# Kernel tuning notes

Measured on AMD Instinct MI355X. Metric: run time of the kernel, lower is better.

## Reference

```python
import jax, jax.numpy as jnp
import numpy as np
from jax import lax

V_PATCH = (1, 4, 16, 64, 256, 1024)  # must end at L
RESI = 0.5    # quant_resi ratio inside Phi
BETA = 0.25
K_PHI = 4     # share_quant_resi


def _phi_indices():
    # PhiPartiallyShared tick lookup, resolved statically per scale
    K = K_PHI
    ticks = np.linspace(1/3/K, 1 - 1/3/K, K) if K == 4 else np.linspace(1/2/K, 1 - 1/2/K, K)
    SN = len(V_PATCH)
    return [int(np.argmin(np.abs(ticks - (si / (SN - 1) if SN > 1 else 0.0)))) for si in range(SN)]


def interp_linear(x, Lo):
    # torch F.interpolate(mode='linear', align_corners=False) on last axis of [B,C,Li]
    Li = x.shape[-1]
    if Li == Lo:
        return x
    pos = (jnp.arange(Lo, dtype=jnp.float32) + 0.5) * (Li / Lo) - 0.5
    pos = jnp.clip(pos, 0.0, Li - 1)
    lo = jnp.floor(pos).astype(jnp.int32)
    hi = jnp.minimum(lo + 1, Li - 1)
    w = pos - lo.astype(jnp.float32)
    return x[..., lo] * (1.0 - w) + x[..., hi] * w


def phi_apply(h, w, b):
    # Phi: h*(1-r) + Conv1d(ks=3,pad=1)(h)*r
    y = lax.conv_general_dilated(h, w, (1,), [(1, 1)], dimension_numbers=('NCH', 'OIH', 'NCH'))
    y = y + b[None, :, None]
    return h * (1.0 - RESI) + y * RESI


def reference(f_BCL, emb, phi_w, phi_b):
    f = f_BCL.astype(jnp.float32)
    B, C, L = f.shape
    f_ng = lax.stop_gradient(f)
    f_rest = f_ng
    f_hat = jnp.zeros_like(f_ng)
    SN = len(V_PATCH)
    pidx = _phi_indices()
    e_sq = jnp.sum(emb * emb, axis=1)  # [V]
    loss = jnp.float32(0.0)
    for si, pl in enumerate(V_PATCH):
        rest = interp_linear(f_rest, pl) if si != SN - 1 else f_rest
        z = rest.transpose(0, 2, 1).reshape(-1, C)              # [B*pl, C]
        d = jnp.sum(z * z, axis=1, keepdims=True) + e_sq - 2.0 * (z @ emb.T)  # [B*pl, V]
        idx = jnp.argmin(d, axis=1)
        h = emb[idx].reshape(B, pl, C).transpose(0, 2, 1)        # [B,C,pl]
        if si != SN - 1:
            h = interp_linear(h, L)
        h = phi_apply(h, phi_w[pidx[si]], phi_b[pidx[si]])
        f_hat = f_hat + h
        f_rest = f_rest - h
        loss = loss + BETA * jnp.mean((lax.stop_gradient(f_hat) - f) ** 2) \
                    + jnp.mean((f_hat - f_ng) ** 2)
    loss = loss / SN
    # straight-through estimator
    f_hat_st = lax.stop_gradient(f_hat) - f_ng + f
    return f_hat_st, loss


def setup_inputs() -> dict:
    key = jax.random.key(0)
    k1, k2, k3 = jax.random.split(key, 3)
    B, C, L, V = 32, 32, 1024, 4096
    f_BCL = jax.random.normal(k1, (B, C, L), dtype=jnp.float32)
    emb = jax.random.normal(k2, (V, C), dtype=jnp.float32)
    phi_w = jax.random.normal(k3, (K_PHI, C, C, 3), dtype=jnp.float32) * 0.05
    phi_b = jnp.zeros((K_PHI, C), dtype=jnp.float32)
    return {"f_BCL": f_BCL, "emb": emb, "phi_w": phi_w, "phi_b": phi_b}
```

## Files before the change

### kernel.cpp

```cpp
#include <hip/hip_runtime.h>
#include <stdint.h>

#define BDIM 32
#define CDIM 32
#define LDIM 1024
#define VDIM 4096
#define BCL (BDIM*CDIM*LDIM)

typedef _Float16 f16x8 __attribute__((ext_vector_type(8)));
typedef float f32x4 __attribute__((ext_vector_type(4)));

#define PIN_V(x) asm volatile("" : "+v"(x))

__device__ __forceinline__ unsigned long long pack_key(float bd, int bv) {
    unsigned u = __float_as_uint(bd);
    u = (u & 0x80000000u) ? ~u : (u | 0x80000000u);
    return ((unsigned long long)u << 32) | (unsigned)bv;
}

__global__ void init_kernel(const float* __restrict__ f, const float* __restrict__ emb,
                            float* __restrict__ f_rest, float* __restrict__ f_hat,
                            float* __restrict__ e_sq, float* __restrict__ loss_acc,
                            unsigned* __restrict__ done_ctr,
                            unsigned long long* __restrict__ keys, int nkeys) {
    int i = blockIdx.x * blockDim.x + threadIdx.x;
    if (i < BCL) { f_rest[i] = f[i]; f_hat[i] = 0.0f; }
    if (i < VDIM) {
        const float* e = emb + (size_t)i * CDIM;
        float s = 0.f;
#pragma unroll
        for (int k = 0; k < 32; ++k) { float v = e[k]; s = fmaf(v, v, s); }
        e_sq[i] = s;
    }
    if (i < nkeys) keys[i] = ~0ull;
    if (i == 0) { *loss_acc = 0.f; *done_ctr = 0u; }
}

__global__ __launch_bounds__(256) void vq_small(
    const float* __restrict__ src, const float* __restrict__ emb,
    _Float16* __restrict__ eh, _Float16* __restrict__ el, float* __restrict__ e_sq,
    unsigned long long* __restrict__ keys,
    float* __restrict__ loss_acc, unsigned* __restrict__ done_ctr,
    int lpl, int s, int NQ)
{
    const int bid = blockIdx.x, t = threadIdx.x;
    if (bid >= NQ) {
        if (bid == NQ && t == 0) { *loss_acc = 0.f; *done_ctr = 0u; }
        int i = (bid - NQ) * 256 + t;
        if (i < VDIM) {
            const float* e = emb + (size_t)i * 32;
            float ssum = 0.f;
#pragma unroll
            for (int k = 0; k < 32; ++k) {
                float v = e[k];
                ssum = fmaf(v, v, ssum);
                _Float16 h = (_Float16)v;
                float r = v - (float)h;
                eh[(size_t)i*32 + k] = (_Float16)(-2.0f) * h;
                el[(size_t)i*32 + k] = (_Float16)(-2.0f) * (_Float16)r;
            }
            e_sq[i] = ssum;
        }
        return;
    }

    const int pl = 1 << lpl;
    const int q = bid;
    const int b = q >> lpl, j = q & (pl - 1);
    const int col = j * s + (s >> 1) - 1;
    const float* p = src + b * (CDIM * LDIM) + col;
    float z[32];
#pragma unroll
    for (int c = 0; c < 32; ++c) z[c] = 0.5f * (p[c * LDIM] + p[c * LDIM + 1]);

    float bd = 3.4e38f; int bv = 0;
    const int vs = t * 16;
    for (int v = vs; v < vs + 16; ++v) {
        const float* e = emb + (size_t)v * 32;
        float ev[32];
#pragma unroll
        for (int c = 0; c < 32; ++c) ev[c] = e[c];
        float es = 0.f;
#pragma unroll
        for (int c = 0; c < 32; ++c) es = fmaf(ev[c], ev[c], es);
        float a = z[0] * ev[0];
#pragma unroll
        for (int c = 1; c < 32; ++c) a = fmaf(z[c], ev[c], a);
        float d = fmaf(a, -2.0f, es);
        if (d < bd) { bd = d; bv = v; }
    }

    unsigned long long key = pack_key(bd, bv);
#pragma unroll
    for (int m = 1; m < 64; m <<= 1) {
        unsigned long long o = __shfl_xor(key, m, 64); if (o < key) key = o;
    }
    __shared__ unsigned long long redk[4];
    if ((t & 63) == 0) redk[t >> 6] = key;
    __syncthreads();
    if (t == 0) {
        unsigned long long kk = redk[0];
#pragma unroll
        for (int m = 1; m < 4; ++m) if (redk[m] < kk) kk = redk[m];
        keys[q] = kk;
    }
}

__global__ __launch_bounds__(256) void vq_mfma(
    const _Float16* __restrict__ z_hi, const _Float16* __restrict__ z_lo,
    const _Float16* __restrict__ e_hi, const _Float16* __restrict__ e_lo,
    const float* __restrict__ e_sq, unsigned long long* __restrict__ keys,
    int NQ, int VC, int vchunks, int vsub)
{
    const int t = threadIdx.x;
    const int lane = t & 63;
    const int w = t >> 6;
    const int qg = blockIdx.x / vchunks;
    const int vc = blockIdx.x % vchunks;
    const int vb0 = vc * (vsub * VC);

    __shared__ __align__(16) _Float16 eh_ls[256*32];
    __shared__ __align__(16) _Float16 el_ls[256*32];
    __shared__ float esq_ls[256];

    const int fr = lane & 15;
    const int kq = lane >> 4;
    const int qbase = qg*256 + w*64;
    f16x8 ah[4], al[4];
#pragma unroll
    for (int tq = 0; tq < 4; ++tq) {
        int q = qbase + tq*16 + fr;
        ah[tq] = *(const f16x8*)(z_hi + (size_t)q*32 + kq*8);
        al[tq] = *(const f16x8*)(z_lo + (size_t)q*32 + kq*8);
    }

    float bd[4][4]; int bv[4][4];
#pragma unroll
    for (int tq = 0; tq < 4; ++tq)
#pragma unroll
        for (int i = 0; i < 4; ++i) { bd[tq][i] = 3.4e38f; bv[tq][i] = 0; }

    for (int sub = 0; sub < vsub; ++sub) {
        const int vb = vb0 + sub * VC;
        {
            const float4* sH = (const float4*)(e_hi + (size_t)vb*32);
            const float4* sL = (const float4*)(e_lo + (size_t)vb*32);
            float4* dH = (float4*)eh_ls; float4* dL = (float4*)el_ls;
            int n4 = VC * 4;
            for (int x = t; x < n4; x += 256) {
                int row = x >> 2, c = x & 3;
                int ds = row*4 + (c ^ ((row >> 1) & 3));
                dH[ds] = sH[x]; dL[ds] = sL[x];
            }
            for (int v = t; v < VC; v += 256) esq_ls[v] = e_sq[vb + v];
        }
        __syncthreads();

        for (int vt = 0; vt < VC; vt += 16) {
            const int row = vt + fr;
            const int koff = (kq ^ ((row >> 1) & 3)) * 8;
            const f16x8 bh = *(const f16x8*)(eh_ls + (size_t)row*32 + koff);
            const f16x8 bl = *(const f16x8*)(el_ls + (size_t)row*32 + koff);
            float es = esq_ls[row];
            int vg = vb + row;
#pragma unroll
            for (int tq = 0; tq < 4; ++tq) {
                f32x4 acc = {es, es, es, es};
                acc = __builtin_amdgcn_mfma_f32_16x16x32_f16(ah[tq], bh, acc, 0,0,0);
                acc = __builtin_amdgcn_mfma_f32_16x16x32_f16(ah[tq], bl, acc, 0,0,0);
                acc = __builtin_amdgcn_mfma_f32_16x16x32_f16(al[tq], bh, acc, 0,0,0);
#pragma unroll
                for (int i = 0; i < 4; ++i)
                    if (acc[i] < bd[tq][i]) { bd[tq][i] = acc[i]; bv[tq][i] = vg; }
            }
        }
        __syncthreads();
    }

#pragma unroll
    for (int tq = 0; tq < 4; ++tq) {
#pragma unroll
        for (int i = 0; i < 4; ++i) {
            unsigned long long k = pack_key(bd[tq][i], bv[tq][i]);
#pragma unroll
            for (int m = 1; m < 16; m <<= 1) {
                unsigned long long o = __shfl_xor(k, m, 64); if (o < k) k = o;
            }
            if (fr == 0) atomicMin(&keys[qbase + tq*16 + kq*4 + i], k);
        }
    }
}

__global__ __launch_bounds__(256) void vq_scan(
    const float* __restrict__ f_rest,
    const float* __restrict__ emb, const float* __restrict__ e_sq,
    unsigned long long* __restrict__ keys,
    int lpl, int s, int NQ, int VC, int vchunks)
{
    const int pl = 1 << lpl;
    const int t  = threadIdx.x;
    const int qg = blockIdx.x / vchunks;
    const int vc = blockIdx.x % vchunks;
    const int vb = vc * VC;

    __shared__ __align__(16) float e_ls[128 * 32];
    __shared__ float esq_ls[128];

    {
        const float4* src = (const float4*)emb + (size_t)vb * 8;
        float4* dst = (float4*)e_ls;
        for (int x = t; x < VC * 8; x += 256) dst[x] = src[x];
        if (t < VC) esq_ls[t] = e_sq[vb + t];
    }

    const int q0 = qg * 512 + t;
    const int q1 = q0 + 256;
    const int qc0 = (q0 < NQ) ? q0 : NQ - 1;
    const int qc1 = (q1 < NQ) ? q1 : NQ - 1;

    float z0[32], z1[32];
    {
        int b0 = qc0 >> lpl, j0 = qc0 & (pl - 1);
        int b1 = qc1 >> lpl, j1 = qc1 & (pl - 1);
        if (pl == LDIM) {
            const float* p0 = f_rest + b0 * (CDIM * LDIM) + j0;
            const float* p1 = f_rest + b1 * (CDIM * LDIM) + j1;
#pragma unroll
            for (int c = 0; c < 32; ++c) { z0[c] = p0[c * LDIM]; z1[c] = p1[c * LDIM]; }
        } else {
            int col0 = j0 * s + (s >> 1) - 1;
            int col1 = j1 * s + (s >> 1) - 1;
            const float* p0 = f_rest + b0 * (CDIM * LDIM) + col0;
            const float* p1 = f_rest + b1 * (CDIM * LDIM) + col1;
#pragma unroll
            for (int c = 0; c < 32; ++c) {
                z0[c] = 0.5f * (p0[c * LDIM] + p0[c * LDIM + 1]);
                z1[c] = 0.5f * (p1[c * LDIM] + p1[c * LDIM + 1]);
            }
        }
    }

    __syncthreads();

    float bd0 = 3.4e38f, bd1 = 3.4e38f;
    int bv0 = 0, bv1 = 0;

#pragma unroll 1
    for (int v = 0; v < VC; v += 2) {
#pragma unroll
        for (int c = 0; c < 32; ++c) { PIN_V(z0[c]); PIN_V(z1[c]); }

        const float4* er0 = (const float4*)&e_ls[(size_t)v * 32];
        const float4* er1 = er0 + 8;
        float es0 = esq_ls[v];
        float es1 = esq_ls[v + 1];

        float4 e0 = er0[0], e1 = er1[0];
        float a00 = z0[0] * e0.x,        a01 = z0[0] * e1.x;
        float a10 = z1[0] * e0.x,        a11 = z1[0] * e1.x;
        a00 = fmaf(z0[1], e0.y, a00);    a01 = fmaf(z0[1], e1.y, a01);
        a10 = fmaf(z1[1], e0.y, a10);    a11 = fmaf(z1[1], e1.y, a11);
        a00 = fmaf(z0[2], e0.z, a00);    a01 = fmaf(z0[2], e1.z, a01);
        a10 = fmaf(z1[2], e0.z, a10);    a11 = fmaf(z1[2], e1.z, a11);
        a00 = fmaf(z0[3], e0.w, a00);    a01 = fmaf(z0[3], e1.w, a01);
        a10 = fmaf(z1[3], e0.w, a10);    a11 = fmaf(z1[3], e1.w, a11);
#pragma unroll
        for (int c4 = 1; c4 < 8; ++c4) {
            e0 = er0[c4]; e1 = er1[c4];
            a00 = fmaf(z0[c4*4+0], e0.x, a00);  a01 = fmaf(z0[c4*4+0], e1.x, a01);
            a10 = fmaf(z1[c4*4+0], e0.x, a10);  a11 = fmaf(z1[c4*4+0], e1.x, a11);
            a00 = fmaf(z0[c4*4+1], e0.y, a00);  a01 = fmaf(z0[c4*4+1], e1.y, a01);
            a10 = fmaf(z1[c4*4+1], e0.y, a10);  a11 = fmaf(z1[c4*4+1], e1.y, a11);
            a00 = fmaf(z0[c4*4+2], e0.z, a00);  a01 = fmaf(z0[c4*4+2], e1.z, a01);
            a10 = fmaf(z1[c4*4+2], e0.z, a10);  a11 = fmaf(z1[c4*4+2], e1.z, a11);
            a00 = fmaf(z0[c4*4+3], e0.w, a00);  a01 = fmaf(z0[c4*4+3], e1.w, a01);
            a10 = fmaf(z1[c4*4+3], e0.w, a10);  a11 = fmaf(z1[c4*4+3], e1.w, a11);
        }
        float d00 = fmaf(a00, -2.0f, es0);
        float d01 = fmaf(a01, -2.0f, es1);
        float d10 = fmaf(a10, -2.0f, es0);
        float d11 = fmaf(a11, -2.0f, es1);
        if (d00 < bd0) { bd0 = d00; bv0 = vb + v; }
        if (d01 < bd0) { bd0 = d01; bv0 = vb + v + 1; }
        if (d10 < bd1) { bd1 = d10; bv1 = vb + v; }
        if (d11 < bd1) { bd1 = d11; bv1 = vb + v + 1; }
    }

    if (q0 < NQ) atomicMin(&keys[q0], pack_key(bd0, bv0));
    if (q1 < NQ) atomicMin(&keys[q1], pack_key(bd1, bv1));
}

__global__ __launch_bounds__(256) void fuse_kernel(
    const float* __restrict__ f, const float* __restrict__ emb,
    const unsigned long long* __restrict__ keys,
    unsigned long long* __restrict__ keys_next, int nq_next,
    _Float16* __restrict__ zh_next, _Float16* __restrict__ zl_next, int s_next,
    const float* __restrict__ w, const float* __restrict__ bias,
    float* __restrict__ f_rest, float* __restrict__ f_hat,
    float* __restrict__ loss_acc, unsigned* __restrict__ done_ctr,
    float* __restrict__ out_loss, int pl, int from_f)
{
    const int t  = threadIdx.x;
    const int b  = blockIdx.y;
    const int l0 = blockIdx.x * 64;

    if (keys_next) {
        int x = (b * gridDim.x + blockIdx.x) * 256 + t;
        if (x < nq_next) keys_next[x] = ~0ull;
    }

    __shared__ float w_s[3072];
    __shared__ float b_s[32];
    __shared__ float hs[32 * 68];
    __shared__ float red[4];
    __shared__ int   v0s[66], v1s[66];
    __shared__ float wgs[66];

    for (int x = t; x < 3072; x += 256) w_s[x] = w[x];
    if (t < 32) b_s[t] = bias[t];

    if (t < 66) {
        int l = l0 - 1 + t;
        if (l < 0 || l >= LDIM) {
            v0s[t] = -1;
        } else {
            int lo, hi; float wg;
            if (pl == LDIM) { lo = l; hi = l; wg = 0.f; }
            else {
                float pos = (l + 0.5f) * ((float)pl / 1024.0f) - 0.5f;
                pos = fminf(fmaxf(pos, 0.f), (float)(pl - 1));
                lo = (int)floorf(pos);
                hi = min(lo + 1, pl - 1);
                wg = pos - (float)lo;
            }
            v0s[t] = (int)(keys[b * pl + lo] & 0xFFFFFFFFull);
            v1s[t] = (int)(keys[b * pl + hi] & 0xFFFFFFFFull);
            wgs[t] = wg;
        }
    }
    __syncthreads();

    for (int x = t; x < 528; x += 256) {
        int cx = x >> 3, i4 = x & 7;
        int v0 = v0s[cx];
        if (v0 < 0) {
            hs[(i4*4+0) * 68 + cx] = 0.f;
            hs[(i4*4+1) * 68 + cx] = 0.f;
            hs[(i4*4+2) * 68 + cx] = 0.f;
            hs[(i4*4+3) * 68 + cx] = 0.f;
        } else {
            float4 a = ((const float4*)(emb + (size_t)v0 * 32))[i4];
            float4 c = ((const float4*)(emb + (size_t)v1s[cx] * 32))[i4];
            float wg = wgs[cx], om = 1.0f - wg;
            hs[(i4*4+0) * 68 + cx] = a.x * om + c.x * wg;
            hs[(i4*4+1) * 68 + cx] = a.y * om + c.y * wg;
            hs[(i4*4+2) * 68 + cx] = a.z * om + c.z * wg;
            hs[(i4*4+3) * 68 + cx] = a.w * om + c.w * wg;
        }
    }
    __syncthreads();

    const int o  = t >> 3;
    const int lg = t & 7;
    const float* wrow = &w_s[o * 96];
    float acc[8];
#pragma unroll
    for (int u = 0; u < 8; ++u) acc[u] = 0.f;
    const int hbase = lg * 8;

#pragma unroll 2
    for (int i = 0; i < 32; ++i) {
        float w0 = wrow[i * 3 + 0], w1 = wrow[i * 3 + 1], w2 = wrow[i * 3 + 2];
        const float* hrow = &hs[i * 68 + hbase];
        float hw[10];
#pragma unroll
        for (int x = 0; x < 10; ++x) hw[x] = hrow[x];
#pragma unroll
        for (int u = 0; u < 8; ++u) {
            acc[u] = fmaf(w0, hw[u], acc[u]);
            acc[u] = fmaf(w1, hw[u + 1], acc[u]);
            acc[u] = fmaf(w2, hw[u + 2], acc[u]);
        }
    }

    float lsum = 0.f;
    float frv[8];
    const int gbase = (b * 32 + o) * LDIM + l0 + lg * 8;
#pragma unroll
    for (int u = 0; u < 8; ++u) {
        float hval = hs[o * 68 + lg * 8 + 1 + u];
        float y = acc[u] + b_s[o];
        float ph = 0.5f * hval + 0.5f * y;
        int gi = gbase + u;
        float fv = f[gi];
        float fh = (from_f ? 0.0f : f_hat[gi]) + ph;
        f_hat[gi] = fh;
        float fr = (from_f ? fv : f_rest[gi]) - ph;
        f_rest[gi] = fr;
        frv[u] = fr;
        float df = fh - fv;
        lsum = fmaf(df, df, lsum);
    }

    if (zh_next) {
        __syncthreads();
#pragma unroll
        for (int u = 0; u < 8; ++u) hs[o * 68 + lg * 8 + u] = frv[u];
        __syncthreads();
        int npos = 64 / s_next;
        int qn_base = b * (LDIM / s_next) + l0 / s_next;
        for (int v = t; v < npos * 32; v += 256) {
            int jl = v >> 5, c = v & 31;
            float zv;
            if (s_next == 1) zv = hs[c * 68 + jl];
            else {
                int cl = jl * s_next + (s_next >> 1) - 1;
                zv = 0.5f * (hs[c * 68 + cl] + hs[c * 68 + cl + 1]);
            }
            _Float16 h = (_Float16)zv;
            float r = zv - (float)h;
            size_t zi = (size_t)(qn_base + jl) * 32 + c;
            zh_next[zi] = h;
            zl_next[zi] = (_Float16)r;
        }
    }

#pragma unroll
    for (int off = 32; off > 0; off >>= 1) lsum += __shfl_down(lsum, off, 64);
    if ((t & 63) == 0) red[t >> 6] = lsum;
    __syncthreads();
    if (t == 0) {
        atomicAdd(loss_acc, red[0] + red[1] + red[2] + red[3]);
        if (out_loss) {
            __threadfence();
            unsigned old = atomicAdd(done_ctr, 1u);
            if (old == (unsigned)(gridDim.x * gridDim.y - 1)) {
                float lv = atomicAdd(loss_acc, 0.0f);
                *out_loss = lv * (1.25f / (6.0f * (float)BCL));
            }
        }
    }
}

extern "C" void kernel_launch(void* const* d_in, const int* in_sizes, int n_in,
                              void* d_out, int out_size, void* d_ws, size_t ws_size,
                              hipStream_t stream)
{
    const float* f    = (const float*)d_in[0];
    const float* emb  = (const float*)d_in[1];
    const float* phiw = (const float*)d_in[2];
    const float* phib = (const float*)d_in[3];

    float* f_hat    = (float*)d_out;
    float* out_loss = f_hat + BCL;

    const int pls[6]   = {1, 4, 16, 64, 256, 1024};
    const int lpls[6]  = {0, 2, 4, 6, 8, 10};
    const int vchm[6]  = {0, 0, 64, 16, 8, 4};
    const int vsbm[6]  = {0, 0, 1, 1, 2, 4};
    const int pidx[6]  = {0, 0, 1, 2, 3, 3};
    const int snx[6]   = {256, 64, 16, 4, 1, 0};

    char* ws = (char*)d_ws;
    float* f_rest = (float*)ws;

    size_t base = (size_t)BCL * 4;
    size_t off = base;
    unsigned long long* keysA = (unsigned long long*)(ws + off);
    unsigned long long* keysB = keysA + 32768;
    off += (size_t)65536 * 8;
    _Float16* z_hi = (_Float16*)(ws + off); off += (size_t)32768 * 32 * 2;
    _Float16* z_lo = (_Float16*)(ws + off); off += (size_t)32768 * 32 * 2;
    _Float16* e_hi = (_Float16*)(ws + off); off += (size_t)VDIM * 32 * 2;
    _Float16* e_lo = (_Float16*)(ws + off); off += (size_t)VDIM * 32 * 2;
    size_t need_mf = off + (size_t)VDIM * 4 + 64;
    bool mf = ws_size >= need_mf;

    if (mf) {
        float* e_sq        = (float*)(ws + off);
        float* loss_acc    = e_sq + VDIM;
        unsigned* done_ctr = (unsigned*)(loss_acc + 1);

        for (int si = 0; si < 6; ++si) {
            int pl = pls[si], s = LDIM / pl, NQ = BDIM * pl;
            unsigned long long* k  = (si & 1) ? keysB : keysA;
            unsigned long long* kn = (si >= 1 && si < 5) ? ((si & 1) ? keysA : keysB) : nullptr;
            int nq_next = (si < 5) ? BDIM * pls[si + 1] : 0;

            if (si <= 1) {
                int grid = NQ + (si == 0 ? 16 : 0);
                vq_small<<<dim3(grid), 256, 0, stream>>>(
                    (si == 0) ? f : f_rest, emb, e_hi, e_lo, e_sq, k,
                    loss_acc, done_ctr, lpls[si], s, NQ);
            } else {
                int vcm = vchm[si], vsb = vsbm[si];
                int VC = VDIM / (vcm * vsb);
                vq_mfma<<<dim3((NQ / 256) * vcm), 256, 0, stream>>>(
                    z_hi, z_lo, e_hi, e_lo, e_sq, k, NQ, VC, vcm, vsb);
            }

            bool zw = (si >= 1 && si <= 4);
            fuse_kernel<<<dim3(16, 32), 256, 0, stream>>>(
                f, emb, k, kn, nq_next,
                zw ? z_hi : nullptr, zw ? z_lo : nullptr, snx[si],
                phiw + (size_t)pidx[si] * 3072, phib + (size_t)pidx[si] * 32,
                f_rest, f_hat, loss_acc, done_ctr,
                (si == 5) ? out_loss : nullptr, pl, (si == 0) ? 1 : 0);
        }
        return;
    }

    {
        const int vch[6]  = {64, 64, 64, 64, 32, 32};
        off = base;
        size_t need_pp = base + (size_t)65536 * 8 + (size_t)VDIM * 4 + 64;
        bool pp = ws_size >= need_pp;
        keysB = pp ? keysA + 32768 : keysA;
        off += pp ? (size_t)65536 * 8 : (size_t)32768 * 8;
        float* e_sq        = (float*)(ws + off);
        float* loss_acc    = e_sq + VDIM;
        unsigned* done_ctr = (unsigned*)(loss_acc + 1);

        init_kernel<<<dim3((BCL + 255) / 256), 256, 0, stream>>>(
            f, emb, f_rest, f_hat, e_sq, loss_acc, done_ctr, keysA, 32768);

        for (int si = 0; si < 6; ++si) {
            int pl = pls[si], s = LDIM / pl, NQ = BDIM * pl;
            int qgroups = (NQ + 511) >> 9;
            int VC = VDIM / vch[si];
            unsigned long long* k  = (si & 1) ? keysB : keysA;
            unsigned long long* kn = (si < 5 && pp) ? ((si & 1) ? keysA : keysB) : nullptr;
            int nq_next = (si < 5) ? BDIM * pls[si + 1] : 0;
            if (!pp && si > 0) hipMemsetAsync(k, 0xFF, (size_t)NQ * 8, stream);
            vq_scan<<<dim3(qgroups * vch[si]), 256, 0, stream>>>(
                f_rest, emb, e_sq, k, lpls[si], s, NQ, VC, vch[si]);
            fuse_kernel<<<dim3(16, 32), 256, 0, stream>>>(
                f, emb, k, kn, nq_next, nullptr, nullptr, snx[si],
                phiw + (size_t)pidx[si] * 3072, phib + (size_t)pidx[si] * 32,
                f_rest, f_hat, loss_acc, done_ctr,
                (si == 5) ? out_loss : nullptr, pl, 0);
        }
    }
}
```

Baseline: 332.1 us.

## Drop f_hat tracking via f-minus-residual identity and shrink fuse tile

Stops carrying f_hat through every scale. The code now relies on f_hat = f - f_rest, so the loss uses the residual squared, and f_hat is written only once in the final scale instead of being read and written at every scale. The fuse kernel is templated on chunk width, and most scales use 16-column chunks with a 4x larger grid for more parallelism. The fallback path replaces vq_scan with vq_small. In exchange, the narrower tiles reload weights per block and add halo overhead, and the loss now relies on the algebraic identity holding in float arithmetic.

```diff
diff --git a/kernel.cpp b/kernel.cpp
--- a/kernel.cpp
+++ b/kernel.cpp
@@ -19,12 +19,12 @@
 }
 
 __global__ void init_kernel(const float* __restrict__ f, const float* __restrict__ emb,
-                            float* __restrict__ f_rest, float* __restrict__ f_hat,
+                            float* __restrict__ f_rest,
                             float* __restrict__ e_sq, float* __restrict__ loss_acc,
                             unsigned* __restrict__ done_ctr,
                             unsigned long long* __restrict__ keys, int nkeys) {
     int i = blockIdx.x * blockDim.x + threadIdx.x;
-    if (i < BCL) { f_rest[i] = f[i]; f_hat[i] = 0.0f; }
+    if (i < BCL) f_rest[i] = f[i];
     if (i < VDIM) {
         const float* e = emb + (size_t)i * CDIM;
         float s = 0.f;
@@ -191,105 +191,7 @@
     }
 }
 
-__global__ __launch_bounds__(256) void vq_scan(
-    const float* __restrict__ f_rest,
-    const float* __restrict__ emb, const float* __restrict__ e_sq,
-    unsigned long long* __restrict__ keys,
-    int lpl, int s, int NQ, int VC, int vchunks)
-{
-    const int pl = 1 << lpl;
-    const int t  = threadIdx.x;
-    const int qg = blockIdx.x / vchunks;
-    const int vc = blockIdx.x % vchunks;
-    const int vb = vc * VC;
-
-    __shared__ __align__(16) float e_ls[128 * 32];
-    __shared__ float esq_ls[128];
-
-    {
-        const float4* src = (const float4*)emb + (size_t)vb * 8;
-        float4* dst = (float4*)e_ls;
-        for (int x = t; x < VC * 8; x += 256) dst[x] = src[x];
-        if (t < VC) esq_ls[t] = e_sq[vb + t];
-    }
-
-    const int q0 = qg * 512 + t;
-    const int q1 = q0 + 256;
-    const int qc0 = (q0 < NQ) ? q0 : NQ - 1;
-    const int qc1 = (q1 < NQ) ? q1 : NQ - 1;
-
-    float z0[32], z1[32];
-    {
-        int b0 = qc0 >> lpl, j0 = qc0 & (pl - 1);
-        int b1 = qc1 >> lpl, j1 = qc1 & (pl - 1);
-        if (pl == LDIM) {
-            const float* p0 = f_rest + b0 * (CDIM * LDIM) + j0;
-            const float* p1 = f_rest + b1 * (CDIM * LDIM) + j1;
-#pragma unroll
-            for (int c = 0; c < 32; ++c) { z0[c] = p0[c * LDIM]; z1[c] = p1[c * LDIM]; }
-        } else {
-            int col0 = j0 * s + (s >> 1) - 1;
-            int col1 = j1 * s + (s >> 1) - 1;
-            const float* p0 = f_rest + b0 * (CDIM * LDIM) + col0;
-            const float* p1 = f_rest + b1 * (CDIM * LDIM) + col1;
-#pragma unroll
-            for (int c = 0; c < 32; ++c) {
-                z0[c] = 0.5f * (p0[c * LDIM] + p0[c * LDIM + 1]);
-                z1[c] = 0.5f * (p1[c * LDIM] + p1[c * LDIM + 1]);
-            }
-        }
-    }
-
-    __syncthreads();
-
-    float bd0 = 3.4e38f, bd1 = 3.4e38f;
-    int bv0 = 0, bv1 = 0;
-
-#pragma unroll 1
-    for (int v = 0; v < VC; v += 2) {
-#pragma unroll
-        for (int c = 0; c < 32; ++c) { PIN_V(z0[c]); PIN_V(z1[c]); }
-
-        const float4* er0 = (const float4*)&e_ls[(size_t)v * 32];
-        const float4* er1 = er0 + 8;
-        float es0 = esq_ls[v];
-        float es1 = esq_ls[v + 1];
-
-        float4 e0 = er0[0], e1 = er1[0];
-        float a00 = z0[0] * e0.x,        a01 = z0[0] * e1.x;
-        float a10 = z1[0] * e0.x,        a11 = z1[0] * e1.x;
-        a00 = fmaf(z0[1], e0.y, a00);    a01 = fmaf(z0[1], e1.y, a01);
-        a10 = fmaf(z1[1], e0.y, a10);    a11 = fmaf(z1[1], e1.y, a11);
-        a00 = fmaf(z0[2], e0.z, a00);    a01 = fmaf(z0[2], e1.z, a01);
-        a10 = fmaf(z1[2], e0.z, a10);    a11 = fmaf(z1[2], e1.z, a11);
-        a00 = fmaf(z0[3], e0.w, a00);    a01 = fmaf(z0[3], e1.w, a01);
-        a10 = fmaf(z1[3], e0.w, a10);    a11 = fmaf(z1[3], e1.w, a11);
-#pragma unroll
-        for (int c4 = 1; c4 < 8; ++c4) {
-            e0 = er0[c4]; e1 = er1[c4];
-            a00 = fmaf(z0[c4*4+0], e0.x, a00);  a01 = fmaf(z0[c4*4+0], e1.x, a01);
-            a10 = fmaf(z1[c4*4+0], e0.x, a10);  a11 = fmaf(z1[c4*4+0], e1.x, a11);
-            a00 = fmaf(z0[c4*4+1], e0.y, a00);  a01 = fmaf(z0[c4*4+1], e1.y, a01);
-            a10 = fmaf(z1[c4*4+1], e0.y, a10);  a11 = fmaf(z1[c4*4+1], e1.y, a11);
-            a00 = fmaf(z0[c4*4+2], e0.z, a00);  a01 = fmaf(z0[c4*4+2], e1.z, a01);
-            a10 = fmaf(z1[c4*4+2], e0.z, a10);  a11 = fmaf(z1[c4*4+2], e1.z, a11);
-            a00 = fmaf(z0[c4*4+3], e0.w, a00);  a01 = fmaf(z0[c4*4+3], e1.w, a01);
-            a10 = fmaf(z1[c4*4+3], e0.w, a10);  a11 = fmaf(z1[c4*4+3], e1.w, a11);
-        }
-        float d00 = fmaf(a00, -2.0f, es0);
-        float d01 = fmaf(a01, -2.0f, es1);
-        float d10 = fmaf(a10, -2.0f, es0);
-        float d11 = fmaf(a11, -2.0f, es1);
-        if (d00 < bd0) { bd0 = d00; bv0 = vb + v; }
-        if (d01 < bd0) { bd0 = d01; bv0 = vb + v + 1; }
-        if (d10 < bd1) { bd1 = d10; bv1 = vb + v; }
-        if (d11 < bd1) { bd1 = d11; bv1 = vb + v + 1; }
-    }
-
-    if (q0 < NQ) atomicMin(&keys[q0], pack_key(bd0, bv0));
-    if (q1 < NQ) atomicMin(&keys[q1], pack_key(bd1, bv1));
-}
-
+template<int CHUNK>
 __global__ __launch_bounds__(256) void fuse_kernel(
     const float* __restrict__ f, const float* __restrict__ emb,
     const unsigned long long* __restrict__ keys,
@@ -298,11 +200,14 @@
     const float* __restrict__ w, const float* __restrict__ bias,
     float* __restrict__ f_rest, float* __restrict__ f_hat,
     float* __restrict__ loss_acc, unsigned* __restrict__ done_ctr,
-    float* __restrict__ out_loss, int pl, int from_f)
+    float* __restrict__ out_loss, int pl, int from_f, int to_hat)
 {
+    constexpr int COLS = CHUNK + 2;
+    constexpr int STR  = CHUNK + 4;
+    constexpr int LPT  = CHUNK / 8;
     const int t  = threadIdx.x;
     const int b  = blockIdx.y;
-    const int l0 = blockIdx.x * 64;
+    const int l0 = blockIdx.x * CHUNK;
 
     if (keys_next) {
         int x = (b * gridDim.x + blockIdx.x) * 256 + t;
@@ -311,15 +216,15 @@
 
     __shared__ float w_s[3072];
     __shared__ float b_s[32];
-    __shared__ float hs[32 * 68];
+    __shared__ float hs[32 * STR];
     __shared__ float red[4];
-    __shared__ int   v0s[66], v1s[66];
-    __shared__ float wgs[66];
+    __shared__ int   v0s[COLS], v1s[COLS];
+    __shared__ float wgs[COLS];
 
     for (int x = t; x < 3072; x += 256) w_s[x] = w[x];
     if (t < 32) b_s[t] = bias[t];
 
-    if (t < 66) {
+    if (t < COLS) {
         int l = l0 - 1 + t;
         if (l < 0 || l >= LDIM) {
             v0s[t] = -1;
@@ -340,22 +245,22 @@
     }
     __syncthreads();
 
-    for (int x = t; x < 528; x += 256) {
+    for (int x = t; x < COLS * 8; x += 256) {
         int cx = x >> 3, i4 = x & 7;
         int v0 = v0s[cx];
         if (v0 < 0) {
-            hs[(i4*4+0) * 68 + cx] = 0.f;
-            hs[(i4*4+1) * 68 + cx] = 0.f;
-            hs[(i4*4+2) * 68 + cx] = 0.f;
-            hs[(i4*4+3) * 68 + cx] = 0.f;
+            hs[(i4*4+0) * STR + cx] = 0.f;
+            hs[(i4*4+1) * STR + cx] = 0.f;
+            hs[(i4*4+2) * STR + cx] = 0.f;
+            hs[(i4*4+3) * STR + cx] = 0.f;
         } else {
             float4 a = ((const float4*)(emb + (size_t)v0 * 32))[i4];
             float4 c = ((const float4*)(emb + (size_t)v1s[cx] * 32))[i4];
             float wg = wgs[cx], om = 1.0f - wg;
-            hs[(i4*4+0) * 68 + cx] = a.x * om + c.x * wg;
-            hs[(i4*4+1) * 68 + cx] = a.y * om + c.y * wg;
-            hs[(i4*4+2) * 68 + cx] = a.z * om + c.z * wg;
-            hs[(i4*4+3) * 68 + cx] = a.w * om + c.w * wg;
+            hs[(i4*4+0) * STR + cx] = a.x * om + c.x * wg;
+            hs[(i4*4+1) * STR + cx] = a.y * om + c.y * wg;
+            hs[(i4*4+2) * STR + cx] = a.z * om + c.z * wg;
+            hs[(i4*4+3) * STR + cx] = a.w * om + c.w * wg;
         }
     }
     __syncthreads();
@@ -363,20 +268,20 @@
     const int o  = t >> 3;
     const int lg = t & 7;
     const float* wrow = &w_s[o * 96];
-    float acc[8];
-#pragma unroll
-    for (int u = 0; u < 8; ++u) acc[u] = 0.f;
-    const int hbase = lg * 8;
+    float acc[LPT];
+#pragma unroll
+    for (int u = 0; u < LPT; ++u) acc[u] = 0.f;
+    const int hbase = lg * LPT;
 
 #pragma unroll 2
     for (int i = 0; i < 32; ++i) {
         float w0 = wrow[i * 3 + 0], w1 = wrow[i * 3 + 1], w2 = wrow[i * 3 + 2];
-        const float* hrow = &hs[i * 68 + hbase];
-        float hw[10];
-#pragma unroll
-        for (int x = 0; x < 10; ++x) hw[x] = hrow[x];
-#pragma unroll
-        for (int u = 0; u < 8; ++u) {
+        const float* hrow = &hs[i * STR + hbase];
+        float hw[LPT + 2];
+#pragma unroll
+        for (int x = 0; x < LPT + 2; ++x) hw[x] = hrow[x];
+#pragma unroll
+        for (int u = 0; u < LPT; ++u) {
             acc[u] = fmaf(w0, hw[u], acc[u]);
             acc[u] = fmaf(w1, hw[u + 1], acc[u]);
             acc[u] = fmaf(w2, hw[u + 2], acc[u]);
@@ -384,38 +289,35 @@
     }
 
     float lsum = 0.f;
-    float frv[8];
-    const int gbase = (b * 32 + o) * LDIM + l0 + lg * 8;
-#pragma unroll
-    for (int u = 0; u < 8; ++u) {
-        float hval = hs[o * 68 + lg * 8 + 1 + u];
+    float frv[LPT];
+    const int gbase = (b * 32 + o) * LDIM + l0 + lg * LPT;
+#pragma unroll
+    for (int u = 0; u < LPT; ++u) {
+        float hval = hs[o * STR + lg * LPT + 1 + u];
         float y = acc[u] + b_s[o];
         float ph = 0.5f * hval + 0.5f * y;
         int gi = gbase + u;
-        float fv = f[gi];
-        float fh = (from_f ? 0.0f : f_hat[gi]) + ph;
-        f_hat[gi] = fh;
-        float fr = (from_f ? fv : f_rest[gi]) - ph;
-        f_rest[gi] = fr;
+        float fr = (from_f ? f[gi] : f_rest[gi]) - ph;
+        if (to_hat) f_hat[gi] = f[gi] - fr;
+        else        f_rest[gi] = fr;
         frv[u] = fr;
-        float df = fh - fv;
-        lsum = fmaf(df, df, lsum);
+        lsum = fmaf(fr, fr, lsum);
     }
 
     if (zh_next) {
         __syncthreads();
 #pragma unroll
-        for (int u = 0; u < 8; ++u) hs[o * 68 + lg * 8 + u] = frv[u];
+        for (int u = 0; u < LPT; ++u) hs[o * STR + lg * LPT + u] = frv[u];
         __syncthreads();
-        int npos = 64 / s_next;
+        int npos = CHUNK / s_next;
         int qn_base = b * (LDIM / s_next) + l0 / s_next;
         for (int v = t; v < npos * 32; v += 256) {
             int jl = v >> 5, c = v & 31;
             float zv;
-            if (s_next == 1) zv = hs[c * 68 + jl];
+            if (s_next == 1) zv = hs[c * STR + jl];
             else {
                 int cl = jl * s_next + (s_next >> 1) - 1;
-                zv = 0.5f * (hs[c * 68 + cl] + hs[c * 68 + cl + 1]);
+                zv = 0.5f * (hs[c * STR + cl] + hs[c * STR + cl + 1]);
             }
             _Float16 h = (_Float16)zv;
             float r = zv - (float)h;
@@ -500,18 +402,28 @@
             }
 
             bool zw = (si >= 1 && si <= 4);
-            fuse_kernel<<<dim3(16, 32), 256, 0, stream>>>(
-                f, emb, k, kn, nq_next,
-                zw ? z_hi : nullptr, zw ? z_lo : nullptr, snx[si],
-                phiw + (size_t)pidx[si] * 3072, phib + (size_t)pidx[si] * 32,
-                f_rest, f_hat, loss_acc, done_ctr,
-                (si == 5) ? out_loss : nullptr, pl, (si == 0) ? 1 : 0);
+            _Float16* zh = zw ? z_hi : nullptr;
+            _Float16* zl = zw ? z_lo : nullptr;
+            const float* wsi = phiw + (size_t)pidx[si] * 3072;
+            const float* bsi = phib + (size_t)pidx[si] * 32;
+            int from_f = (si == 0) ? 1 : 0;
+            int to_hat = (si == 5) ? 1 : 0;
+            float* ol = (si == 5) ? out_loss : nullptr;
+
+            if (si == 1) {
+                fuse_kernel<64><<<dim3(16, 32), 256, 0, stream>>>(
+                    f, emb, k, kn, nq_next, zh, zl, snx[si], wsi, bsi,
+                    f_rest, f_hat, loss_acc, done_ctr, ol, pl, from_f, to_hat);
+            } else {
+                fuse_kernel<16><<<dim3(64, 32), 256, 0, stream>>>(
+                    f, emb, k, kn, nq_next, zh, zl, snx[si], wsi, bsi,
+                    f_rest, f_hat, loss_acc, done_ctr, ol, pl, from_f, to_hat);
+            }
         }
         return;
     }
 
     {
-        const int vch[6]  = {64, 64, 64, 64, 32, 32};
         off = base;
         size_t need_pp = base + (size_t)65536 * 8 + (size_t)VDIM * 4 + 64;
         bool pp = ws_size >= need_pp;
@@ -522,23 +434,22 @@
         unsigned* done_ctr = (unsigned*)(loss_acc + 1);
 
         init_kernel<<<dim3((BCL + 255) / 256), 256, 0, stream>>>(
-            f, emb, f_rest, f_hat, e_sq, loss_acc, done_ctr, keysA, 32768);
+            f, emb, f_rest, e_sq, loss_acc, done_ctr, keysA, 32768);
 
         for (int si = 0; si < 6; ++si) {
             int pl = pls[si], s = LDIM / pl, NQ = BDIM * pl;
-            int qgroups = (NQ + 511) >> 9;
-            int VC = VDIM / vch[si];
             unsigned long long* k  = (si & 1) ? keysB : keysA;
             unsigned long long* kn = (si < 5 && pp) ? ((si & 1) ? keysA : keysB) : nullptr;
             int nq_next = (si < 5) ? BDIM * pls[si + 1] : 0;
             if (!pp && si > 0) hipMemsetAsync(k, 0xFF, (size_t)NQ * 8, stream);
-            vq_scan<<<dim3(qgroups * vch[si]), 256, 0, stream>>>(
-                f_rest, emb, e_sq, k, lpls[si], s, NQ, VC, vch[si]);
-            fuse_kernel<<<dim3(16, 32), 256, 0, stream>>>(
+            vq_small<<<dim3(NQ), 256, 0, stream>>>(
+                (si == 0) ? f : f_rest, emb, nullptr, nullptr, e_sq, k,
+                loss_acc, done_ctr, lpls[si], s, NQ);
+            fuse_kernel<64><<<dim3(16, 32), 256, 0, stream>>>(
                 f, emb, k, kn, nq_next, nullptr, nullptr, snx[si],
                 phiw + (size_t)pidx[si] * 3072, phib + (size_t)pidx[si] * 32,
                 f_rest, f_hat, loss_acc, done_ctr,
-                (si == 5) ? out_loss : nullptr, pl, 0);
-        }
-    }
-}
+                (si == 5) ? out_loss : nullptr, pl, (si == 0) ? 1 : 0, (si == 5) ? 1 : 0);
+        }
+    }
+}
```

Result: slower. 400.0 us (+20.4%).
